# Performance work log

Measured on AMD Instinct MI355X. Metric: run time of the kernel, lower is better.

The kernel has to match this reference:

```python
import jax, jax.numpy as jnp
import numpy as np

INPUT_SCALE = 1.0
TABLE_SIZE = 32
D_EMBED = 64
N = 1_000_000


def setup_inputs() -> dict:
    key = jax.random.key(0)
    k1, k2 = jax.random.split(key)
    x = jax.random.normal(k1, (N, 3), dtype=jnp.float32)
    # learned table parameter: [E, D, H, W] (batch dim of 1 dropped)
    table = jax.random.normal(k2, (D_EMBED, TABLE_SIZE, TABLE_SIZE, TABLE_SIZE), dtype=jnp.float32) * 0.1
    return {"x": x, "table": table}


def _grid_sample_3d(table, grid):
    """F.grid_sample(table[None], grid[None,None,None]) with mode='bilinear',
    padding_mode='zeros', align_corners=False.
    table: [E, D, H, W]; grid: [n, 3] with (x->W, y->H, z->D) order.
    Returns [n, E]."""
    E, Dz, Hy, Wx = table.shape
    sizes_f = jnp.array([Wx, Hy, Dz], dtype=table.dtype)
    dims_i = jnp.array([Wx, Hy, Dz], dtype=jnp.int32)
    # align_corners=False: pix = ((coord + 1) * size - 1) / 2
    pix = ((grid + 1.0) * sizes_f - 1.0) * 0.5   # [n, 3]
    p0f = jnp.floor(pix)
    frac = pix - p0f                              # [n, 3]
    p0 = p0f.astype(jnp.int32)
    tab_flat = table.reshape(E, -1).T             # [D*H*W, E]
    out = jnp.zeros((grid.shape[0], E), dtype=table.dtype)
    for dz in (0, 1):
        for dy in (0, 1):
            for dx in (0, 1):
                off = jnp.array([dx, dy, dz], dtype=jnp.int32)
                idx = p0 + off                                        # [n, 3]
                inb = jnp.all((idx >= 0) & (idx < dims_i), axis=-1)   # zeros padding
                idxc = jnp.clip(idx, 0, dims_i - 1)
                lin = (idxc[:, 2] * Hy + idxc[:, 1]) * Wx + idxc[:, 0]
                vals = tab_flat[lin]                                  # [n, E]
                w = jnp.prod(jnp.where(off == 1, frac, 1.0 - frac), axis=-1)
                out = out + vals * (w * inb.astype(table.dtype))[:, None]
    return out


def reference(x, table):
    xc = jnp.clip(x * INPUT_SCALE, -1.0, 1.0)
    return _grid_sample_3d(table, xc)
```

## Files before the change

kernel.cpp:

```cpp
#include <hip/hip_runtime.h>


constexpr int TSZ = 32;
constexpr int S   = TSZ * TSZ * TSZ;
constexpr int EMB = 64;

typedef float floatx4 __attribute__((ext_vector_type(4)));

__device__ __forceinline__ unsigned short f32_to_bf16_rne(float f) {
  unsigned int u = __float_as_uint(f);
  unsigned int lsb = (u >> 16) & 1u;
  u += 0x7FFFu + lsb;
  return (unsigned short)(u >> 16);
}

__global__ __launch_bounds__(256) void transpose_table_k(
    const float* __restrict__ tab, unsigned short* __restrict__ tabT) {
  __shared__ float tile[EMB][EMB + 1];
  const int s_base = blockIdx.x * 64;
  const int t  = threadIdx.x;
  const int c0 = t & 63;
  const int r0 = t >> 6;
#pragma unroll
  for (int i = 0; i < 16; ++i) {
    const int e = r0 + 4 * i;
    tile[e][c0] = tab[(size_t)e * S + (s_base + c0)];
  }
  __syncthreads();
#pragma unroll
  for (int i = 0; i < 16; ++i) {
    const int s = r0 + 4 * i;
    tabT[(size_t)(s_base + s) * EMB + c0] = f32_to_bf16_rne(tile[c0][s]);
  }
}

__global__ __launch_bounds__(256) void embed_k(
    const float* __restrict__ x, const uint4* __restrict__ tabT,
    float* __restrict__ out, int n) {
  const int gid = blockIdx.x * 256 + threadIdx.x;
  const int pt  = gid >> 3;
  if (pt >= n) return;
  const int c8 = gid & 7;

  const float gx = fminf(fmaxf(__builtin_nontemporal_load(&x[3 * pt + 0]), -1.f), 1.f);
  const float gy = fminf(fmaxf(__builtin_nontemporal_load(&x[3 * pt + 1]), -1.f), 1.f);
  const float gz = fminf(fmaxf(__builtin_nontemporal_load(&x[3 * pt + 2]), -1.f), 1.f);
  const float px = ((gx + 1.f) * 32.f - 1.f) * 0.5f;
  const float py = ((gy + 1.f) * 32.f - 1.f) * 0.5f;
  const float pz = ((gz + 1.f) * 32.f - 1.f) * 0.5f;

  const float fxf = floorf(px), fyf = floorf(py), fzf = floorf(pz);
  const int ix0 = (int)fxf, iy0 = (int)fyf, iz0 = (int)fzf;
  const float fx = px - fxf, fy = py - fyf, fz = pz - fzf;
  const float wx[2] = {1.f - fx, fx};
  const float wy[2] = {1.f - fy, fy};
  const float wz[2] = {1.f - fz, fz};

  float acc[8];
#pragma unroll
  for (int k = 0; k < 8; ++k) acc[k] = 0.f;

#pragma unroll
  for (int dz = 0; dz < 2; ++dz) {
    const int  iz  = iz0 + dz;
    const bool bz  = (unsigned)iz < (unsigned)TSZ;
    const int  izc = min(max(iz, 0), TSZ - 1);
#pragma unroll
    for (int dy = 0; dy < 2; ++dy) {
      const int  iy  = iy0 + dy;
      const bool by  = (unsigned)iy < (unsigned)TSZ;
      const int  iyc = min(max(iy, 0), TSZ - 1);
      const int  rowbase = (izc * TSZ + iyc) * TSZ;
      const float wzy = wz[dz] * wy[dy];
#pragma unroll
      for (int dx = 0; dx < 2; ++dx) {
        const int  ix  = ix0 + dx;
        const bool bx  = (unsigned)ix < (unsigned)TSZ;
        const int  ixc = min(max(ix, 0), TSZ - 1);
        float w = wzy * wx[dx];
        w = (bx && by && bz) ? w : 0.f;
        const int lin = rowbase + ixc;
        const uint4 q = tabT[lin * 8 + c8];
        const float v0 = __uint_as_float(q.x << 16);
        const float v1 = __uint_as_float(q.x & 0xFFFF0000u);
        const float v2 = __uint_as_float(q.y << 16);
        const float v3 = __uint_as_float(q.y & 0xFFFF0000u);
        const float v4 = __uint_as_float(q.z << 16);
        const float v5 = __uint_as_float(q.z & 0xFFFF0000u);
        const float v6 = __uint_as_float(q.w << 16);
        const float v7 = __uint_as_float(q.w & 0xFFFF0000u);
        acc[0] = fmaf(w, v0, acc[0]);
        acc[1] = fmaf(w, v1, acc[1]);
        acc[2] = fmaf(w, v2, acc[2]);
        acc[3] = fmaf(w, v3, acc[3]);
        acc[4] = fmaf(w, v4, acc[4]);
        acc[5] = fmaf(w, v5, acc[5]);
        acc[6] = fmaf(w, v6, acc[6]);
        acc[7] = fmaf(w, v7, acc[7]);
      }
    }
  }

  const floatx4 s0 = {acc[0], acc[1], acc[2], acc[3]};
  const floatx4 s1 = {acc[4], acc[5], acc[6], acc[7]};
  floatx4* dst = (floatx4*)(out + (size_t)pt * EMB + c8 * 8);
  __builtin_nontemporal_store(s0, &dst[0]);
  __builtin_nontemporal_store(s1, &dst[1]);
}

__global__ __launch_bounds__(256) void embed_fallback_k(
    const float* __restrict__ x, const float* __restrict__ tab,
    float* __restrict__ out, int n) {
  const int gid = blockIdx.x * 256 + threadIdx.x;
  const int pt  = gid >> 6;
  if (pt >= n) return;
  const int e = gid & 63;

  const float gx = fminf(fmaxf(x[3 * pt + 0], -1.f), 1.f);
  const float gy = fminf(fmaxf(x[3 * pt + 1], -1.f), 1.f);
  const float gz = fminf(fmaxf(x[3 * pt + 2], -1.f), 1.f);
  const float px = ((gx + 1.f) * 32.f - 1.f) * 0.5f;
  const float py = ((gy + 1.f) * 32.f - 1.f) * 0.5f;
  const float pz = ((gz + 1.f) * 32.f - 1.f) * 0.5f;

  const float fxf = floorf(px), fyf = floorf(py), fzf = floorf(pz);
  const int ix0 = (int)fxf, iy0 = (int)fyf, iz0 = (int)fzf;
  const float fx = px - fxf, fy = py - fyf, fz = pz - fzf;
  const float wx[2] = {1.f - fx, fx};
  const float wy[2] = {1.f - fy, fy};
  const float wz[2] = {1.f - fz, fz};

  float acc = 0.f;
#pragma unroll
  for (int dz = 0; dz < 2; ++dz) {
    const int  iz  = iz0 + dz;
    const bool bz  = (unsigned)iz < (unsigned)TSZ;
    const int  izc = min(max(iz, 0), TSZ - 1);
#pragma unroll
    for (int dy = 0; dy < 2; ++dy) {
      const int  iy  = iy0 + dy;
      const bool by  = (unsigned)iy < (unsigned)TSZ;
      const int  iyc = min(max(iy, 0), TSZ - 1);
#pragma unroll
      for (int dx = 0; dx < 2; ++dx) {
        const int  ix  = ix0 + dx;
        const bool bx  = (unsigned)ix < (unsigned)TSZ;
        const int  ixc = min(max(ix, 0), TSZ - 1);
        float w = wz[dz] * wy[dy] * wx[dx];
        w = (bx && by && bz) ? w : 0.f;
        const int lin = (izc * TSZ + iyc) * TSZ + ixc;
        acc = fmaf(w, tab[(size_t)e * S + lin], acc);
      }
    }
  }
  out[(size_t)pt * EMB + e] = acc;
}

extern "C" void kernel_launch(void* const* d_in, const int* in_sizes, int n_in,
                              void* d_out, int out_size, void* d_ws,
                              size_t ws_size, hipStream_t stream) {
  const float* x   = (const float*)d_in[0];
  const float* tab = (const float*)d_in[1];
  float*       out = (float*)d_out;
  const int n = in_sizes[0] / 3;

  const size_t need = (size_t)S * EMB * sizeof(unsigned short);
  if (ws_size >= need) {
    unsigned short* tabT = (unsigned short*)d_ws;
    transpose_table_k<<<S / 64, 256, 0, stream>>>(tab, tabT);
    const int total  = n * 8;
    const int blocks = (total + 255) / 256;
    embed_k<<<blocks, 256, 0, stream>>>(x, (const uint4*)tabT, out, n);
  } else {
    const int total  = n * EMB;
    const int blocks = (total + 255) / 256;
    embed_fallback_k<<<blocks, 256, 0, stream>>>(x, tab, out, n);
  }
}
```

Measured before the change: 319.1 us.

## Split bf16 table into channel halves and interleave half-specific blocks across XCDs

```diff
diff --git a/kernel.cpp b/kernel.cpp
--- a/kernel.cpp
+++ b/kernel.cpp
@@ -6,6 +6,7 @@
 constexpr int EMB = 64;
 
 typedef float floatx4 __attribute__((ext_vector_type(4)));
+typedef float f32x2   __attribute__((ext_vector_type(2)));
 
 __device__ __forceinline__ unsigned short f32_to_bf16_rne(float f) {
   unsigned int u = __float_as_uint(f);
@@ -27,20 +28,27 @@
     tile[e][c0] = tab[(size_t)e * S + (s_base + c0)];
   }
   __syncthreads();
+  const int hv = c0 >> 5;
+  const int ch = c0 & 31;
 #pragma unroll
   for (int i = 0; i < 16; ++i) {
     const int s = r0 + 4 * i;
-    tabT[(size_t)(s_base + s) * EMB + c0] = f32_to_bf16_rne(tile[c0][s]);
+    tabT[(size_t)hv * S * 32 + (size_t)(s_base + s) * 32 + ch] =
+        f32_to_bf16_rne(tile[c0][s]);
   }
 }
 
 __global__ __launch_bounds__(256) void embed_k(
     const float* __restrict__ x, const uint4* __restrict__ tabT,
-    float* __restrict__ out, int n) {
-  const int gid = blockIdx.x * 256 + threadIdx.x;
-  const int pt  = gid >> 3;
+    float* __restrict__ out, int n, int nchunks) {
+  const int bid = blockIdx.x;
+  const int hv    = (bid >> 2) & 1;
+  const int chunk = (bid >> 3) * 4 + (bid & 3);
+  if (chunk >= nchunks) return;
+  const int t  = threadIdx.x;
+  const int pt = chunk * 64 + (t >> 2);
   if (pt >= n) return;
-  const int c8 = gid & 7;
+  const int o  = t & 3;
 
   const float gx = fminf(fmaxf(__builtin_nontemporal_load(&x[3 * pt + 0]), -1.f), 1.f);
   const float gy = fminf(fmaxf(__builtin_nontemporal_load(&x[3 * pt + 1]), -1.f), 1.f);
@@ -52,60 +60,60 @@
   const float fxf = floorf(px), fyf = floorf(py), fzf = floorf(pz);
   const int ix0 = (int)fxf, iy0 = (int)fyf, iz0 = (int)fzf;
   const float fx = px - fxf, fy = py - fyf, fz = pz - fzf;
-  const float wx[2] = {1.f - fx, fx};
-  const float wy[2] = {1.f - fy, fy};
-  const float wz[2] = {1.f - fz, fz};
 
-  float acc[8];
-#pragma unroll
-  for (int k = 0; k < 8; ++k) acc[k] = 0.f;
+  float wxe[2], wye[2], wze[2];
+  int   ixc[2], iyc[2], izc[2];
+  wxe[0] = (ix0 >= 0)       ? (1.f - fx) : 0.f;
+  wxe[1] = (ix0 + 1 < TSZ)  ? fx         : 0.f;
+  ixc[0] = max(ix0, 0);
+  ixc[1] = min(ix0 + 1, TSZ - 1);
+  wye[0] = (iy0 >= 0)       ? (1.f - fy) : 0.f;
+  wye[1] = (iy0 + 1 < TSZ)  ? fy         : 0.f;
+  iyc[0] = max(iy0, 0);
+  iyc[1] = min(iy0 + 1, TSZ - 1);
+  wze[0] = (iz0 >= 0)       ? (1.f - fz) : 0.f;
+  wze[1] = (iz0 + 1 < TSZ)  ? fz         : 0.f;
+  izc[0] = max(iz0, 0);
+  izc[1] = min(iz0 + 1, TSZ - 1);
+
+  const uint4* tb = tabT + (size_t)hv * (S * 4);
+
+  f32x2 a01 = {0.f, 0.f}, a23 = {0.f, 0.f}, a45 = {0.f, 0.f}, a67 = {0.f, 0.f};
 
 #pragma unroll
   for (int dz = 0; dz < 2; ++dz) {
-    const int  iz  = iz0 + dz;
-    const bool bz  = (unsigned)iz < (unsigned)TSZ;
-    const int  izc = min(max(iz, 0), TSZ - 1);
+    const int zb = izc[dz] * (TSZ * TSZ);
 #pragma unroll
     for (int dy = 0; dy < 2; ++dy) {
-      const int  iy  = iy0 + dy;
-      const bool by  = (unsigned)iy < (unsigned)TSZ;
-      const int  iyc = min(max(iy, 0), TSZ - 1);
-      const int  rowbase = (izc * TSZ + iyc) * TSZ;
-      const float wzy = wz[dz] * wy[dy];
+      const int   zyb = zb + iyc[dy] * TSZ;
+      const float wzy = wze[dz] * wye[dy];
 #pragma unroll
       for (int dx = 0; dx < 2; ++dx) {
-        const int  ix  = ix0 + dx;
-        const bool bx  = (unsigned)ix < (unsigned)TSZ;
-        const int  ixc = min(max(ix, 0), TSZ - 1);
-        float w = wzy * wx[dx];
-        w = (bx && by && bz) ? w : 0.f;
-        const int lin = rowbase + ixc;
-        const uint4 q = tabT[lin * 8 + c8];
-        const float v0 = __uint_as_float(q.x << 16);
-        const float v1 = __uint_as_float(q.x & 0xFFFF0000u);
-        const float v2 = __uint_as_float(q.y << 16);
-        const float v3 = __uint_as_float(q.y & 0xFFFF0000u);
-        const float v4 = __uint_as_float(q.z << 16);
-        const float v5 = __uint_as_float(q.z & 0xFFFF0000u);
-        const float v6 = __uint_as_float(q.w << 16);
-        const float v7 = __uint_as_float(q.w & 0xFFFF0000u);
-        acc[0] = fmaf(w, v0, acc[0]);
-        acc[1] = fmaf(w, v1, acc[1]);
-        acc[2] = fmaf(w, v2, acc[2]);
-        acc[3] = fmaf(w, v3, acc[3]);
-        acc[4] = fmaf(w, v4, acc[4]);
-        acc[5] = fmaf(w, v5, acc[5]);
-        acc[6] = fmaf(w, v6, acc[6]);
-        acc[7] = fmaf(w, v7, acc[7]);
+        const float w   = wzy * wxe[dx];
+        const int   lin = zyb + ixc[dx];
+        const uint4 q   = tb[lin * 4 + o];
+        const f32x2 w2  = {w, w};
+        const f32x2 v01 = {__uint_as_float(q.x << 16),
+                           __uint_as_float(q.x & 0xFFFF0000u)};
+        const f32x2 v23 = {__uint_as_float(q.y << 16),
+                           __uint_as_float(q.y & 0xFFFF0000u)};
+        const f32x2 v45 = {__uint_as_float(q.z << 16),
+                           __uint_as_float(q.z & 0xFFFF0000u)};
+        const f32x2 v67 = {__uint_as_float(q.w << 16),
+                           __uint_as_float(q.w & 0xFFFF0000u)};
+        a01 = __builtin_elementwise_fma(v01, w2, a01);
+        a23 = __builtin_elementwise_fma(v23, w2, a23);
+        a45 = __builtin_elementwise_fma(v45, w2, a45);
+        a67 = __builtin_elementwise_fma(v67, w2, a67);
       }
     }
   }
 
-  const floatx4 s0 = {acc[0], acc[1], acc[2], acc[3]};
-  const floatx4 s1 = {acc[4], acc[5], acc[6], acc[7]};
-  floatx4* dst = (floatx4*)(out + (size_t)pt * EMB + c8 * 8);
-  __builtin_nontemporal_store(s0, &dst[0]);
-  __builtin_nontemporal_store(s1, &dst[1]);
+  const floatx4 s0 = {a01.x, a01.y, a23.x, a23.y};
+  const floatx4 s1 = {a45.x, a45.y, a67.x, a67.y};
+  float* dstp = out + (size_t)pt * EMB + hv * 32 + o * 8;
+  __builtin_nontemporal_store(s0, (floatx4*)dstp);
+  __builtin_nontemporal_store(s1, (floatx4*)(dstp + 4));
 }
 
 __global__ __launch_bounds__(256) void embed_fallback_k(
@@ -168,9 +176,9 @@
   if (ws_size >= need) {
     unsigned short* tabT = (unsigned short*)d_ws;
     transpose_table_k<<<S / 64, 256, 0, stream>>>(tab, tabT);
-    const int total  = n * 8;
-    const int blocks = (total + 255) / 256;
-    embed_k<<<blocks, 256, 0, stream>>>(x, (const uint4*)tabT, out, n);
+    const int C = (n + 63) / 64;
+    const int G = ((2 * C + 7) / 8) * 8;
+    embed_k<<<G, 256, 0, stream>>>(x, (const uint4*)tabT, out, n, C);
   } else {
     const int total  = n * EMB;
     const int blocks = (total + 255) / 256;
```

After: 336.8 us. 1.06x slower.
